# Kernel optimization log

Hardware: AMD Instinct MI355X
Metric: run time of the kernel (lower is better)

Reference implementation:

```python
import jax, jax.numpy as jnp
import numpy as np

INPUT_SIZE, OUTPUT_SIZE, HIDDEN, NUM_LAYERS, T = 32, 10, 1536, 2, 64


def _lstm_cell(x, h, c, W_ih, W_hh, b_ih, b_hh):
    # PyTorch LSTMCell: gates ordered i, f, g, o
    g = x @ W_ih.T + b_ih + h @ W_hh.T + b_hh
    i_, f_, g_, o_ = jnp.split(g, 4, axis=-1)
    c2 = jax.nn.sigmoid(f_) * c + jax.nn.sigmoid(i_) * jnp.tanh(g_)
    h2 = jax.nn.sigmoid(o_) * jnp.tanh(c2)
    return h2, c2


def setup_inputs() -> dict:
    key = jax.random.key(0)
    ks = jax.random.split(key, 16)
    s = 1.0 / np.sqrt(HIDDEN)
    u = lambda k, shape: jax.random.uniform(k, shape, jnp.float32, -s, s)
    return {
        "inputs": jax.random.normal(ks[0], (T, 1, INPUT_SIZE), jnp.float32),
        "h_init": jnp.zeros((NUM_LAYERS, 1, HIDDEN), jnp.float32),
        "c_init": jnp.zeros((NUM_LAYERS, 1, HIDDEN), jnp.float32),
        "W_ih0": u(ks[1], (4 * HIDDEN, INPUT_SIZE)),
        "W_hh0": u(ks[2], (4 * HIDDEN, HIDDEN)),
        "b_ih0": u(ks[3], (4 * HIDDEN,)),
        "b_hh0": u(ks[4], (4 * HIDDEN,)),
        "W_ih1": u(ks[5], (4 * HIDDEN, HIDDEN)),
        "W_hh1": u(ks[6], (4 * HIDDEN, HIDDEN)),
        "b_ih1": u(ks[7], (4 * HIDDEN,)),
        "b_hh1": u(ks[8], (4 * HIDDEN,)),
        "W_lin": u(ks[9], (OUTPUT_SIZE, HIDDEN)),
        "b_lin": u(ks[10], (OUTPUT_SIZE,)),
        "lookup": jnp.asarray(np.linspace(0.1, 1.0, OUTPUT_SIZE), jnp.float32),
    }


def reference(inputs, h_init, c_init, W_ih0, W_hh0, b_ih0, b_hh0,
              W_ih1, W_hh1, b_ih1, b_hh1, W_lin, b_lin, lookup):
    S = T * INPUT_SIZE  # total sequential sub-steps
    keys = jax.random.split(jax.random.key(42), S)
    iidx = jnp.arange(S) // INPUT_SIZE  # timestep index
    jidx = jnp.arange(S) % INPUT_SIZE   # feature sub-step index
    pos = jnp.arange(INPUT_SIZE)

    def step(carry, xs):
        h0, c0, h1, c1, x_aug = carry
        k, i, j = xs
        # fresh input at the start of each timestep (j == 0)
        x = jnp.where(j == 0, inputs[i], x_aug)  # [1, INPUT_SIZE]
        h0, c0 = _lstm_cell(x, h0, c0, W_ih0, W_hh0, b_ih0, b_hh0)
        h1, c1 = _lstm_cell(h0, h1, c1, W_ih1, W_hh1, b_ih1, b_hh1)
        logits = h1 @ W_lin.T + b_lin          # [1, OUTPUT_SIZE]
        probs = jax.nn.softmax(logits, -1)
        action = jax.random.categorical(k, logits, axis=-1)  # [1] int
        scale = jnp.where(j == 0, 1.0, lookup[action])        # [1]
        # mult: ones except position j scaled by lookup[action]
        new_x = x * jnp.where(pos[None, :] == j, scale[:, None], 1.0)
        return (h0, c0, h1, c1, new_x), (action, probs)

    carry0 = (h_init[0], c_init[0], h_init[1], c_init[1], inputs[0])
    _, (actions, probs) = jax.lax.scan(step, carry0, (keys, iidx, jidx))
    return actions, probs  # [S,1] int, [S,1,OUTPUT_SIZE] float
```

## Files before the change

kernel.cpp:

```cpp
#include <hip/hip_runtime.h>
#include <math.h>

#define NWG   256
#define TPB   512
#define H     1536
#define S_TOT 2048
#define RPW   6
#define GRW   24
#define OUTP  2048

struct Params {
  const float* __restrict__ inputs; const float* __restrict__ h_init;
  const float* __restrict__ c_init;
  const float* __restrict__ W_ih0; const float* __restrict__ W_hh0;
  const float* __restrict__ b_ih0; const float* __restrict__ b_hh0;
  const float* __restrict__ W_ih1; const float* __restrict__ W_hh1;
  const float* __restrict__ b_ih1; const float* __restrict__ b_hh1;
  const float* __restrict__ W_lin; const float* __restrict__ b_lin;
  const float* __restrict__ lookup;
  float* __restrict__ out; float* __restrict__ h0g; float* __restrict__ h1g;
  unsigned* __restrict__ bar;
};

__device__ __forceinline__ float gload(const float* p) {
  return __hip_atomic_load(p, __ATOMIC_RELAXED, __HIP_MEMORY_SCOPE_AGENT);
}
__device__ __forceinline__ void gstore(float* p, float v) {
  __hip_atomic_store(p, v, __ATOMIC_RELAXED, __HIP_MEMORY_SCOPE_AGENT);
}

__device__ __forceinline__ void tf2x32(unsigned k0, unsigned k1,
                                       unsigned x0, unsigned x1,
                                       unsigned& o0, unsigned& o1) {
  unsigned ks2 = k0 ^ k1 ^ 0x1BD11BDAu;
  x0 += k0; x1 += k1;
#define TFR(r) { x0 += x1; x1 = ((x1 << r) | (x1 >> (32 - r))); x1 ^= x0; }
  TFR(13) TFR(15) TFR(26) TFR(6)   x0 += k1;  x1 += ks2 + 1u;
  TFR(17) TFR(29) TFR(16) TFR(24)  x0 += ks2; x1 += k0 + 2u;
  TFR(13) TFR(15) TFR(26) TFR(6)   x0 += k0;  x1 += k1 + 3u;
  TFR(17) TFR(29) TFR(16) TFR(24)  x0 += k1;  x1 += ks2 + 4u;
  TFR(13) TFR(15) TFR(26) TFR(6)   x0 += ks2; x1 += k0 + 5u;
#undef TFR
  o0 = x0; o1 = x1;
}

__device__ __forceinline__ double bsum64(double v) {
#pragma unroll
  for (int o = 32; o > 0; o >>= 1) v += __shfl_xor(v, o);
  return v;
}

__device__ __forceinline__ float sigf(float x) { return 1.0f / (1.0f + expf(-x)); }

__device__ __forceinline__ void flagbar(unsigned* bar, unsigned e, int tid, int wg) {
  __builtin_amdgcn_fence(__ATOMIC_RELEASE, "agent");
  __syncthreads();
  if (tid == 0)
    __hip_atomic_store(&bar[wg], e, __ATOMIC_RELEASE, __HIP_MEMORY_SCOPE_AGENT);
  if (tid < 64) {
    const unsigned* f = bar + tid * 4;
    bool done;
    do {
      int d0 = (int)(__hip_atomic_load(f + 0, __ATOMIC_RELAXED, __HIP_MEMORY_SCOPE_AGENT) - e);
      int d1 = (int)(__hip_atomic_load(f + 1, __ATOMIC_RELAXED, __HIP_MEMORY_SCOPE_AGENT) - e);
      int d2 = (int)(__hip_atomic_load(f + 2, __ATOMIC_RELAXED, __HIP_MEMORY_SCOPE_AGENT) - e);
      int d3 = (int)(__hip_atomic_load(f + 3, __ATOMIC_RELAXED, __HIP_MEMORY_SCOPE_AGENT) - e);
      done = ((d0 | d1 | d2 | d3) >= 0);
    } while (!__all(done));
    __builtin_amdgcn_fence(__ATOMIC_ACQUIRE, "agent");
  }
  __syncthreads();
}

__device__ __forceinline__ void cntbar(unsigned* cnt, unsigned target, int tid) {
  __builtin_amdgcn_fence(__ATOMIC_RELEASE, "agent");
  __syncthreads();
  if (tid == 0)
    (void)__hip_atomic_fetch_add(cnt, 1u, __ATOMIC_RELEASE, __HIP_MEMORY_SCOPE_AGENT);
  if (tid < 64) {
    for (;;) {
      unsigned c = __hip_atomic_load(cnt, __ATOMIC_RELAXED, __HIP_MEMORY_SCOPE_AGENT);
      if ((int)(c - target) >= 0) break;
      __builtin_amdgcn_s_sleep(4);
    }
    __builtin_amdgcn_fence(__ATOMIC_ACQUIRE, "agent");
  }
  __syncthreads();
}

__global__ __launch_bounds__(TPB)
__attribute__((amdgpu_num_vgpr(256)))
void lstm_persistent(Params P) {
  const int tid  = threadIdx.x;
  const int wg   = blockIdx.x;
  const int wv   = tid >> 6;
  const int lane = tid & 63;

  __shared__ float s_Wlin[10 * H];
  __shared__ float s_W3[8 * H];
  __shared__ float s_Wih0[GRW * 32];
  __shared__ float s_h0[H], s_h1[H];
  __shared__ float s_bih0[GRW], s_bhh0[GRW], s_bih1[GRW], s_bhh1[GRW];
  __shared__ float s_hh1dot[GRW], s_gate[GRW];
  __shared__ float s_x[32];
  __shared__ float s_c0[RPW], s_c1[RPW];
  __shared__ float s_logits[16];
  __shared__ float s_blin[10], s_lookup[10];
  __shared__ int   s_action;

  unsigned* cnt = P.bar + 512;

  if (wg == 0 && tid == 0)
    __hip_atomic_store(cnt, 0u, __ATOMIC_RELAXED, __HIP_MEMORY_SCOPE_AGENT);
  for (int k = tid; k < GRW * 32; k += TPB) {
    int idx = k >> 5, kk = k & 31;
    int q = idx / RPW, u = idx % RPW;
    int gr = q * H + wg * RPW + u;
    s_Wih0[k] = P.W_ih0[gr * 32 + kk];
  }
  for (int k = tid; k < 10 * H; k += TPB) s_Wlin[k] = P.W_lin[k];
  for (int k = tid; k < 8 * H; k += TPB) {
    int w8 = k / H, col = k % H;
    int idx = w8 * 3 + 2;
    int q = idx / RPW, u = idx % RPW;
    int gr = q * H + wg * RPW + u;
    s_W3[k] = P.W_ih1[(size_t)gr * H + col];
  }
  if (tid < GRW) {
    int q = tid / RPW, u = tid % RPW;
    int gr = q * H + wg * RPW + u;
    s_bih0[tid] = P.b_ih0[gr]; s_bhh0[tid] = P.b_hh0[gr];
    s_bih1[tid] = P.b_ih1[gr]; s_bhh1[tid] = P.b_hh1[gr];
  }
  if (tid < 10) { s_blin[tid] = P.b_lin[tid]; s_lookup[tid] = P.lookup[tid]; }
  if (tid < RPW) {
    s_c0[tid] = P.c_init[wg * RPW + tid];
    s_c1[tid] = P.c_init[H + wg * RPW + tid];
    gstore(P.h0g + wg * RPW + tid, P.h_init[wg * RPW + tid]);
    gstore(P.h1g + wg * RPW + tid, P.h_init[H + wg * RPW + tid]);
  }

  float wr[8][24];
#pragma unroll
  for (int slot = 0; slot < 3; ++slot) {
    int idx = wv * 3 + slot;
    int q = idx / RPW, u = idx % RPW;
    int gr = q * H + wg * RPW + u;
    const float* r0 = P.W_hh0 + (size_t)gr * H;
    const float* r1 = P.W_hh1 + (size_t)gr * H;
#pragma unroll
    for (int t = 0; t < 24; ++t) {
      int off = lane + (t << 6);
      wr[slot][t] = r0[off]; wr[3 + slot][t] = r1[off];
    }
  }
#pragma unroll
  for (int slot = 0; slot < 2; ++slot) {
    int idx = wv * 3 + slot;
    int q = idx / RPW, u = idx % RPW;
    int gr = q * H + wg * RPW + u;
    const float* r2 = P.W_ih1 + (size_t)gr * H;
#pragma unroll
    for (int t = 0; t < 24; ++t) wr[6 + slot][t] = r2[lane + (t << 6)];
  }

  flagbar(P.bar, 1u, tid, wg);
  unsigned bt = 0;

  for (int s = 0; s <= S_TOT; ++s) {
#pragma unroll
    for (int r = 0; r < 3; ++r) {
      int k = tid + r * TPB;
      s_h0[k] = gload(P.h0g + k);
      s_h1[k] = gload(P.h1g + k);
    }
    __syncthreads();

    if (s > 0) {
      int sp = s - 1;
#pragma unroll
      for (int p2 = 0; p2 < 2; ++p2) {
        int l = wv + 8 * p2;
        if (l < 10) {
          double acc = 0.0;
#pragma unroll
          for (int t = 0; t < 24; ++t) {
            int off = lane + (t << 6);
            acc += (double)s_Wlin[l * H + off] * (double)s_h1[off];
          }
          acc = bsum64(acc);
          if (lane == 0) s_logits[l] = __fadd_rn((float)acc, s_blin[l]);
        }
      }
      __syncthreads();

      if (wv == 0) {
        unsigned kk0, kk1; tf2x32(0u, 42u, 0u, (unsigned)sp, kk0, kk1);
        unsigned b1, b2; tf2x32(kk0, kk1, 0u, (unsigned)lane, b1, b2);
        unsigned bits = b1 ^ b2;
        float uraw = __fsub_rn(__uint_as_float((bits >> 9) | 0x3F800000u), 1.0f);
        const float TINY = 1.17549435e-38f;
        float u  = fmaxf(TINY, __fadd_rn(uraw, TINY));
        float gum = -logf(-logf(u));
        float lg = (lane < 10) ? s_logits[lane] : 0.0f;
        float y  = (lane < 10) ? __fadd_rn(lg, gum) : -INFINITY;
        int ai = lane;
#pragma unroll
        for (int o = 1; o < 16; o <<= 1) {
          float oy = __shfl_xor(y, o); int oi = __shfl_xor(ai, o);
          if (oy > y || (oy == y && oi < ai)) { y = oy; ai = oi; }
        }
        float lm = (lane < 10) ? lg : -INFINITY;
#pragma unroll
        for (int o = 1; o < 16; o <<= 1) lm = fmaxf(lm, __shfl_xor(lm, o));
        float e2 = (lane < 10) ? expf(__fsub_rn(lg, lm)) : 0.0f;
        float ssum = e2;
#pragma unroll
        for (int o = 1; o < 16; o <<= 1) ssum = __fadd_rn(ssum, __shfl_xor(ssum, o));
        if (lane == 0) s_action = ai;
        if (wg == 0) {
          if (lane < 10) P.out[OUTP + sp * 10 + lane] = e2 / ssum;
          if (lane == 0) P.out[sp] = (float)ai;
        }
      }
      __syncthreads();
      if (tid == 0) {
        int jp = sp & 31;
        if (jp != 0) s_x[jp] = __fmul_rn(s_x[jp], s_lookup[s_action]);
      }
      __syncthreads();
    }

    if (s == S_TOT) break;
    int ii = s >> 5, jj = s & 31;
    if (jj == 0 && tid < 32) s_x[tid] = P.inputs[ii * 32 + tid];
    __syncthreads();

    {
      double a0 = 0, a1 = 0, a2 = 0, b0 = 0, b1 = 0, b2 = 0;
#pragma unroll
      for (int t = 0; t < 24; ++t) {
        int off = lane + (t << 6);
        double h0v = (double)s_h0[off];
        double h1v = (double)s_h1[off];
        a0 += (double)wr[0][t] * h0v;
        a1 += (double)wr[1][t] * h0v;
        a2 += (double)wr[2][t] * h0v;
        b0 += (double)wr[3][t] * h1v;
        b1 += (double)wr[4][t] * h1v;
        b2 += (double)wr[5][t] * h1v;
      }
      a0 = bsum64(a0); a1 = bsum64(a1); a2 = bsum64(a2);
      b0 = bsum64(b0); b1 = bsum64(b1); b2 = bsum64(b2);
      double xa[3];
#pragma unroll
      for (int slot = 0; slot < 3; ++slot) {
        int idx = wv * 3 + slot;
        double pp = (lane < 32)
          ? (double)s_Wih0[(idx << 5) + lane] * (double)s_x[lane] : 0.0;
#pragma unroll
        for (int o = 16; o > 0; o >>= 1) pp += __shfl_xor(pp, o);
        xa[slot] = pp;
      }
      if (lane == 0) {
        double aa[3] = {a0, a1, a2}, bb[3] = {b0, b1, b2};
#pragma unroll
        for (int slot = 0; slot < 3; ++slot) {
          int idx = wv * 3 + slot;
          float g0 = __fadd_rn(__fadd_rn(__fadd_rn((float)xa[slot], s_bih0[idx]),
                                         (float)aa[slot]), s_bhh0[idx]);
          s_gate[idx]   = g0;
          s_hh1dot[idx] = (float)bb[slot];
        }
      }
    }
    __syncthreads();
    if (tid < RPW) {
      int u = tid;
      float gi = s_gate[u], gf = s_gate[6 + u], gg = s_gate[12 + u], go = s_gate[18 + u];
      float c = __fadd_rn(__fmul_rn(sigf(gf), s_c0[u]), __fmul_rn(sigf(gi), tanhf(gg)));
      s_c0[u] = c;
      float h = __fmul_rn(sigf(go), tanhf(c));
      gstore(P.h0g + wg * RPW + u, h);
    }
    bt += NWG; cntbar(cnt, bt, tid);

#pragma unroll
    for (int r = 0; r < 3; ++r) {
      int k = tid + r * TPB;
      s_h0[k] = gload(P.h0g + k);
    }
    __syncthreads();
    {
      double a0 = 0, a1 = 0, a2 = 0;
#pragma unroll
      for (int t = 0; t < 24; ++t) {
        int off = lane + (t << 6);
        double hv = (double)s_h0[off];
        a0 += (double)wr[6][t] * hv;
        a1 += (double)wr[7][t] * hv;
        a2 += (double)s_W3[wv * H + off] * hv;
      }
      a0 = bsum64(a0); a1 = bsum64(a1); a2 = bsum64(a2);
      if (lane == 0) {
        double aa[3] = {a0, a1, a2};
#pragma unroll
        for (int slot = 0; slot < 3; ++slot) {
          int idx = wv * 3 + slot;
          s_gate[idx] = __fadd_rn(__fadd_rn(__fadd_rn((float)aa[slot], s_bih1[idx]),
                                            s_hh1dot[idx]), s_bhh1[idx]);
        }
      }
    }
    __syncthreads();
    if (tid < RPW) {
      int u = tid;
      float gi = s_gate[u], gf = s_gate[6 + u], gg = s_gate[12 + u], go = s_gate[18 + u];
      float c = __fadd_rn(__fmul_rn(sigf(gf), s_c1[u]), __fmul_rn(sigf(gi), tanhf(gg)));
      s_c1[u] = c;
      float h = __fmul_rn(sigf(go), tanhf(c));
      gstore(P.h1g + wg * RPW + u, h);
    }
    bt += NWG; cntbar(cnt, bt, tid);
  }
}

extern "C" void kernel_launch(void* const* d_in, const int* in_sizes, int n_in,
                              void* d_out, int out_size, void* d_ws, size_t ws_size,
                              hipStream_t stream) {
  (void)in_sizes; (void)n_in; (void)out_size; (void)ws_size;
  Params p;
  p.inputs = (const float*)d_in[0];
  p.h_init = (const float*)d_in[1];
  p.c_init = (const float*)d_in[2];
  p.W_ih0  = (const float*)d_in[3];
  p.W_hh0  = (const float*)d_in[4];
  p.b_ih0  = (const float*)d_in[5];
  p.b_hh0  = (const float*)d_in[6];
  p.W_ih1  = (const float*)d_in[7];
  p.W_hh1  = (const float*)d_in[8];
  p.b_ih1  = (const float*)d_in[9];
  p.b_hh1  = (const float*)d_in[10];
  p.W_lin  = (const float*)d_in[11];
  p.b_lin  = (const float*)d_in[12];
  p.lookup = (const float*)d_in[13];
  p.out    = (float*)d_out;
  float* ws = (float*)d_ws;
  p.h0g = ws;
  p.h1g = ws + H;
  p.bar = (unsigned*)(ws + 2 * H);

  hipLaunchKernelGGL(lstm_persistent, dim3(NWG), dim3(TPB), 0, stream, p);
}
```

Baseline: 186.5 ms.

## Stream recurrent weights from global memory instead of pinning them in registers

```diff
diff --git a/kernel.cpp b/kernel.cpp
--- a/kernel.cpp
+++ b/kernel.cpp
@@ -89,7 +89,6 @@
 }
 
 __global__ __launch_bounds__(TPB)
-__attribute__((amdgpu_num_vgpr(256)))
 void lstm_persistent(Params P) {
   const int tid  = threadIdx.x;
   const int wg   = blockIdx.x;
@@ -97,7 +96,6 @@
   const int lane = tid & 63;
 
   __shared__ float s_Wlin[10 * H];
-  __shared__ float s_W3[8 * H];
   __shared__ float s_Wih0[GRW * 32];
   __shared__ float s_h0[H], s_h1[H];
   __shared__ float s_bih0[GRW], s_bhh0[GRW], s_bih1[GRW], s_bhh1[GRW];
@@ -119,13 +117,6 @@
     s_Wih0[k] = P.W_ih0[gr * 32 + kk];
   }
   for (int k = tid; k < 10 * H; k += TPB) s_Wlin[k] = P.W_lin[k];
-  for (int k = tid; k < 8 * H; k += TPB) {
-    int w8 = k / H, col = k % H;
-    int idx = w8 * 3 + 2;
-    int q = idx / RPW, u = idx % RPW;
-    int gr = q * H + wg * RPW + u;
-    s_W3[k] = P.W_ih1[(size_t)gr * H + col];
-  }
   if (tid < GRW) {
     int q = tid / RPW, u = tid % RPW;
     int gr = q * H + wg * RPW + u;
@@ -140,28 +131,21 @@
     gstore(P.h1g + wg * RPW + tid, P.h_init[H + wg * RPW + tid]);
   }
 
-  float wr[8][24];
-#pragma unroll
-  for (int slot = 0; slot < 3; ++slot) {
-    int idx = wv * 3 + slot;
-    int q = idx / RPW, u = idx % RPW;
-    int gr = q * H + wg * RPW + u;
-    const float* r0 = P.W_hh0 + (size_t)gr * H;
-    const float* r1 = P.W_hh1 + (size_t)gr * H;
-#pragma unroll
-    for (int t = 0; t < 24; ++t) {
-      int off = lane + (t << 6);
-      wr[slot][t] = r0[off]; wr[3 + slot][t] = r1[off];
-    }
-  }
-#pragma unroll
-  for (int slot = 0; slot < 2; ++slot) {
-    int idx = wv * 3 + slot;
-    int q = idx / RPW, u = idx % RPW;
-    int gr = q * H + wg * RPW + u;
-    const float* r2 = P.W_ih1 + (size_t)gr * H;
-#pragma unroll
-    for (int t = 0; t < 24; ++t) wr[6 + slot][t] = r2[lane + (t << 6)];
+  const float *r0, *r1, *r2, *r3, *r4, *r5, *r6, *r7, *r8;
+  {
+    int idx0 = wv * 3 + 0, idx1 = wv * 3 + 1, idx2 = wv * 3 + 2;
+    int g0 = (idx0 / RPW) * H + wg * RPW + (idx0 % RPW);
+    int g1 = (idx1 / RPW) * H + wg * RPW + (idx1 % RPW);
+    int g2 = (idx2 / RPW) * H + wg * RPW + (idx2 % RPW);
+    r0 = P.W_hh0 + (size_t)g0 * H;
+    r1 = P.W_hh0 + (size_t)g1 * H;
+    r2 = P.W_hh0 + (size_t)g2 * H;
+    r3 = P.W_hh1 + (size_t)g0 * H;
+    r4 = P.W_hh1 + (size_t)g1 * H;
+    r5 = P.W_hh1 + (size_t)g2 * H;
+    r6 = P.W_ih1 + (size_t)g0 * H;
+    r7 = P.W_ih1 + (size_t)g1 * H;
+    r8 = P.W_ih1 + (size_t)g2 * H;
   }
 
   flagbar(P.bar, 1u, tid, wg);
@@ -243,12 +227,12 @@
         int off = lane + (t << 6);
         double h0v = (double)s_h0[off];
         double h1v = (double)s_h1[off];
-        a0 += (double)wr[0][t] * h0v;
-        a1 += (double)wr[1][t] * h0v;
-        a2 += (double)wr[2][t] * h0v;
-        b0 += (double)wr[3][t] * h1v;
-        b1 += (double)wr[4][t] * h1v;
-        b2 += (double)wr[5][t] * h1v;
+        a0 += (double)r0[off] * h0v;
+        a1 += (double)r1[off] * h0v;
+        a2 += (double)r2[off] * h0v;
+        b0 += (double)r3[off] * h1v;
+        b1 += (double)r4[off] * h1v;
+        b2 += (double)r5[off] * h1v;
       }
       a0 = bsum64(a0); a1 = bsum64(a1); a2 = bsum64(a2);
       b0 = bsum64(b0); b1 = bsum64(b1); b2 = bsum64(b2);
@@ -297,9 +281,9 @@
       for (int t = 0; t < 24; ++t) {
         int off = lane + (t << 6);
         double hv = (double)s_h0[off];
-        a0 += (double)wr[6][t] * hv;
-        a1 += (double)wr[7][t] * hv;
-        a2 += (double)s_W3[wv * H + off] * hv;
+        a0 += (double)r6[off] * hv;
+        a1 += (double)r7[off] * hv;
+        a2 += (double)r8[off] * hv;
       }
       a0 = bsum64(a0); a1 = bsum64(a1); a2 = bsum64(a2);
       if (lane == 0) {
```

Result: slower. 271.3 ms (+45.5%).

## Double workgroup count to halve per-workgroup rows and rebalance weights across waves

Applied to the files above, without the earlier changes.

```diff
diff --git a/kernel.cpp b/kernel.cpp
--- a/kernel.cpp
+++ b/kernel.cpp
@@ -1,12 +1,13 @@
 #include <hip/hip_runtime.h>
 #include <math.h>
 
-#define NWG   256
+#define NWG   512
 #define TPB   512
 #define H     1536
 #define S_TOT 2048
-#define RPW   6
-#define GRW   24
+#define RPW   3
+#define GRW   12
+#define NLW   8
 #define OUTP  2048
 
 struct Params {
@@ -58,14 +59,14 @@
   if (tid == 0)
     __hip_atomic_store(&bar[wg], e, __ATOMIC_RELEASE, __HIP_MEMORY_SCOPE_AGENT);
   if (tid < 64) {
-    const unsigned* f = bar + tid * 4;
+    const unsigned* f = bar + tid * 8;
     bool done;
     do {
-      int d0 = (int)(__hip_atomic_load(f + 0, __ATOMIC_RELAXED, __HIP_MEMORY_SCOPE_AGENT) - e);
-      int d1 = (int)(__hip_atomic_load(f + 1, __ATOMIC_RELAXED, __HIP_MEMORY_SCOPE_AGENT) - e);
-      int d2 = (int)(__hip_atomic_load(f + 2, __ATOMIC_RELAXED, __HIP_MEMORY_SCOPE_AGENT) - e);
-      int d3 = (int)(__hip_atomic_load(f + 3, __ATOMIC_RELAXED, __HIP_MEMORY_SCOPE_AGENT) - e);
-      done = ((d0 | d1 | d2 | d3) >= 0);
+      int dd = 0;
+#pragma unroll
+      for (int i = 0; i < 8; ++i)
+        dd |= (int)(__hip_atomic_load(f + i, __ATOMIC_RELAXED, __HIP_MEMORY_SCOPE_AGENT) - e);
+      done = (dd >= 0);
     } while (!__all(done));
     __builtin_amdgcn_fence(__ATOMIC_ACQUIRE, "agent");
   }
@@ -89,15 +90,14 @@
 }
 
 __global__ __launch_bounds__(TPB)
-__attribute__((amdgpu_num_vgpr(256)))
+__attribute__((amdgpu_waves_per_eu(4)))
 void lstm_persistent(Params P) {
   const int tid  = threadIdx.x;
   const int wg   = blockIdx.x;
   const int wv   = tid >> 6;
   const int lane = tid & 63;
 
-  __shared__ float s_Wlin[10 * H];
-  __shared__ float s_W3[8 * H];
+  __shared__ float s_W1[NLW * H];
   __shared__ float s_Wih0[GRW * 32];
   __shared__ float s_h0[H], s_h1[H];
   __shared__ float s_bih0[GRW], s_bhh0[GRW], s_bih1[GRW], s_bhh1[GRW];
@@ -108,7 +108,7 @@
   __shared__ float s_blin[10], s_lookup[10];
   __shared__ int   s_action;
 
-  unsigned* cnt = P.bar + 512;
+  unsigned* cnt = P.bar + 640;
 
   if (wg == 0 && tid == 0)
     __hip_atomic_store(cnt, 0u, __ATOMIC_RELAXED, __HIP_MEMORY_SCOPE_AGENT);
@@ -118,13 +118,11 @@
     int gr = q * H + wg * RPW + u;
     s_Wih0[k] = P.W_ih0[gr * 32 + kk];
   }
-  for (int k = tid; k < 10 * H; k += TPB) s_Wlin[k] = P.W_lin[k];
-  for (int k = tid; k < 8 * H; k += TPB) {
-    int w8 = k / H, col = k % H;
-    int idx = w8 * 3 + 2;
-    int q = idx / RPW, u = idx % RPW;
+  for (int k = tid; k < NLW * H; k += TPB) {
+    int r = k / H, col = k % H;
+    int q = r / RPW, u = r % RPW;
     int gr = q * H + wg * RPW + u;
-    s_W3[k] = P.W_ih1[(size_t)gr * H + col];
+    s_W1[k] = P.W_ih1[(size_t)gr * H + col];
   }
   if (tid < GRW) {
     int q = tid / RPW, u = tid % RPW;
@@ -140,28 +138,31 @@
     gstore(P.h1g + wg * RPW + tid, P.h_init[H + wg * RPW + tid]);
   }
 
-  float wr[8][24];
-#pragma unroll
-  for (int slot = 0; slot < 3; ++slot) {
-    int idx = wv * 3 + slot;
-    int q = idx / RPW, u = idx % RPW;
-    int gr = q * H + wg * RPW + u;
-    const float* r0 = P.W_hh0 + (size_t)gr * H;
-    const float* r1 = P.W_hh1 + (size_t)gr * H;
-#pragma unroll
-    for (int t = 0; t < 24; ++t) {
-      int off = lane + (t << 6);
-      wr[slot][t] = r0[off]; wr[3 + slot][t] = r1[off];
-    }
-  }
-#pragma unroll
-  for (int slot = 0; slot < 2; ++slot) {
-    int idx = wv * 3 + slot;
-    int q = idx / RPW, u = idx % RPW;
-    int gr = q * H + wg * RPW + u;
-    const float* r2 = P.W_ih1 + (size_t)gr * H;
-#pragma unroll
-    for (int t = 0; t < 24; ++t) wr[6 + slot][t] = r2[lane + (t << 6)];
+  float wrA[3][24];
+  float wrB[24];
+  {
+    const float* srcA = (wv < 4) ? P.W_hh0 : P.W_hh1;
+    int base = (wv < 4) ? wv * 3 : (wv - 4) * 3;
+#pragma unroll
+    for (int sl = 0; sl < 3; ++sl) {
+      int lidx = base + sl;
+      int q = lidx / RPW, u = lidx % RPW;
+      int gr = q * H + wg * RPW + u;
+      const float* rp = srcA + (size_t)gr * H;
+#pragma unroll
+      for (int t = 0; t < 24; ++t) wrA[sl][t] = rp[lane + (t << 6)];
+    }
+    if (wv < 4) {
+      int lidx = 8 + wv;
+      int q = lidx / RPW, u = lidx % RPW;
+      int gr = q * H + wg * RPW + u;
+      const float* rp = P.W_ih1 + (size_t)gr * H;
+#pragma unroll
+      for (int t = 0; t < 24; ++t) wrB[t] = rp[lane + (t << 6)];
+    } else {
+#pragma unroll
+      for (int t = 0; t < 24; ++t) wrB[t] = 0.0f;
+    }
   }
 
   flagbar(P.bar, 1u, tid, wg);
@@ -182,11 +183,12 @@
       for (int p2 = 0; p2 < 2; ++p2) {
         int l = wv + 8 * p2;
         if (l < 10) {
+          const float* wl = P.W_lin + l * H;
           double acc = 0.0;
 #pragma unroll
           for (int t = 0; t < 24; ++t) {
             int off = lane + (t << 6);
-            acc += (double)s_Wlin[l * H + off] * (double)s_h1[off];
+            acc += (double)wl[off] * (double)s_h1[off];
           }
           acc = bsum64(acc);
           if (lane == 0) s_logits[l] = __fadd_rn((float)acc, s_blin[l]);
@@ -237,47 +239,52 @@
     __syncthreads();
 
     {
-      double a0 = 0, a1 = 0, a2 = 0, b0 = 0, b1 = 0, b2 = 0;
+      const float* hp = (wv < 4) ? s_h0 : s_h1;
+      double a0 = 0, a1 = 0, a2 = 0;
 #pragma unroll
       for (int t = 0; t < 24; ++t) {
         int off = lane + (t << 6);
-        double h0v = (double)s_h0[off];
-        double h1v = (double)s_h1[off];
-        a0 += (double)wr[0][t] * h0v;
-        a1 += (double)wr[1][t] * h0v;
-        a2 += (double)wr[2][t] * h0v;
-        b0 += (double)wr[3][t] * h1v;
-        b1 += (double)wr[4][t] * h1v;
-        b2 += (double)wr[5][t] * h1v;
+        double hv = (double)hp[off];
+        a0 += (double)wrA[0][t] * hv;
+        a1 += (double)wrA[1][t] * hv;
+        a2 += (double)wrA[2][t] * hv;
       }
       a0 = bsum64(a0); a1 = bsum64(a1); a2 = bsum64(a2);
-      b0 = bsum64(b0); b1 = bsum64(b1); b2 = bsum64(b2);
-      double xa[3];
-#pragma unroll
-      for (int slot = 0; slot < 3; ++slot) {
-        int idx = wv * 3 + slot;
-        double pp = (lane < 32)
-          ? (double)s_Wih0[(idx << 5) + lane] * (double)s_x[lane] : 0.0;
-#pragma unroll
-        for (int o = 16; o > 0; o >>= 1) pp += __shfl_xor(pp, o);
-        xa[slot] = pp;
-      }
-      if (lane == 0) {
-        double aa[3] = {a0, a1, a2}, bb[3] = {b0, b1, b2};
-#pragma unroll
-        for (int slot = 0; slot < 3; ++slot) {
-          int idx = wv * 3 + slot;
-          float g0 = __fadd_rn(__fadd_rn(__fadd_rn((float)xa[slot], s_bih0[idx]),
-                                         (float)aa[slot]), s_bhh0[idx]);
-          s_gate[idx]   = g0;
-          s_hh1dot[idx] = (float)bb[slot];
+      if (wv < 4) {
+        double xa[3];
+#pragma unroll
+        for (int sl = 0; sl < 3; ++sl) {
+          int d = wv * 3 + sl;
+          double pp = (lane < 32)
+            ? (double)s_Wih0[(d << 5) + lane] * (double)s_x[lane] : 0.0;
+#pragma unroll
+          for (int o = 16; o > 0; o >>= 1) pp += __shfl_xor(pp, o);
+          xa[sl] = pp;
+        }
+        if (lane == 0) {
+          double aa[3] = {a0, a1, a2};
+#pragma unroll
+          for (int sl = 0; sl < 3; ++sl) {
+            int d = wv * 3 + sl;
+            s_gate[d] = __fadd_rn(__fadd_rn(__fadd_rn((float)xa[sl], s_bih0[d]),
+                                            (float)aa[sl]), s_bhh0[d]);
+          }
+        }
+      } else {
+        if (lane == 0) {
+          double aa[3] = {a0, a1, a2};
+#pragma unroll
+          for (int sl = 0; sl < 3; ++sl) {
+            int d = (wv - 4) * 3 + sl;
+            s_hh1dot[d] = (float)aa[sl];
+          }
         }
       }
     }
     __syncthreads();
     if (tid < RPW) {
       int u = tid;
-      float gi = s_gate[u], gf = s_gate[6 + u], gg = s_gate[12 + u], go = s_gate[18 + u];
+      float gi = s_gate[u], gf = s_gate[3 + u], gg = s_gate[6 + u], go = s_gate[9 + u];
       float c = __fadd_rn(__fmul_rn(sigf(gf), s_c0[u]), __fmul_rn(sigf(gi), tanhf(gg)));
       s_c0[u] = c;
       float h = __fmul_rn(sigf(go), tanhf(c));
@@ -292,30 +299,37 @@
     }
     __syncthreads();
     {
-      double a0 = 0, a1 = 0, a2 = 0;
+      double aL = 0;
 #pragma unroll
       for (int t = 0; t < 24; ++t) {
         int off = lane + (t << 6);
-        double hv = (double)s_h0[off];
-        a0 += (double)wr[6][t] * hv;
-        a1 += (double)wr[7][t] * hv;
-        a2 += (double)s_W3[wv * H + off] * hv;
-      }
-      a0 = bsum64(a0); a1 = bsum64(a1); a2 = bsum64(a2);
+        aL += (double)s_W1[wv * H + off] * (double)s_h0[off];
+      }
+      aL = bsum64(aL);
       if (lane == 0) {
-        double aa[3] = {a0, a1, a2};
-#pragma unroll
-        for (int slot = 0; slot < 3; ++slot) {
-          int idx = wv * 3 + slot;
-          s_gate[idx] = __fadd_rn(__fadd_rn(__fadd_rn((float)aa[slot], s_bih1[idx]),
-                                            s_hh1dot[idx]), s_bhh1[idx]);
+        int d = wv;
+        s_gate[d] = __fadd_rn(__fadd_rn(__fadd_rn((float)aL, s_bih1[d]),
+                                        s_hh1dot[d]), s_bhh1[d]);
+      }
+      if (wv < 4) {
+        double aR = 0;
+#pragma unroll
+        for (int t = 0; t < 24; ++t) {
+          int off = lane + (t << 6);
+          aR += (double)wrB[t] * (double)s_h0[off];
+        }
+        aR = bsum64(aR);
+        if (lane == 0) {
+          int d = 8 + wv;
+          s_gate[d] = __fadd_rn(__fadd_rn(__fadd_rn((float)aR, s_bih1[d]),
+                                          s_hh1dot[d]), s_bhh1[d]);
         }
       }
     }
     __syncthreads();
     if (tid < RPW) {
       int u = tid;
-      float gi = s_gate[u], gf = s_gate[6 + u], gg = s_gate[12 + u], go = s_gate[18 + u];
+      float gi = s_gate[u], gf = s_gate[3 + u], gg = s_gate[6 + u], go = s_gate[9 + u];
       float c = __fadd_rn(__fmul_rn(sigf(gf), s_c1[u]), __fmul_rn(sigf(gi), tanhf(gg)));
       s_c1[u] = c;
       float h = __fmul_rn(sigf(go), tanhf(c));
```

Result: slower. 364.2 ms (+95.3%).
